# Performance work log

Hardware: AMD Instinct MI355X
Metric: run time of the kernel (lower is better)

The kernel has to match this reference:

```python
import math
import jax, jax.numpy as jnp
import numpy as np

B, S, D = 1, 2048, 2048
H, KV, HD = 32, 4, 64  # n_heads, n_kv_heads, head_dim
N_REP = H // KV
ROPE_THETA = 10000.0


def setup_inputs() -> dict:
    key = jax.random.key(0)
    ks = jax.random.split(key, 6)
    x = jax.random.normal(ks[0], (B, S, D), dtype=jnp.float32)
    # precomputed rotary frequencies (real/imag parts of freqs_cis)
    inv_freq = 1.0 / (ROPE_THETA ** (jnp.arange(0, HD, 2, dtype=jnp.float32) / HD))  # [HD/2]
    t = jnp.arange(S, dtype=jnp.float32)
    ang = jnp.outer(t, inv_freq)  # [S, HD/2]
    freqs_cos = jnp.cos(ang)
    freqs_sin = jnp.sin(ang)
    # additive causal mask (large negative instead of -inf; numerically equivalent)
    mask = jnp.where(jnp.tril(jnp.ones((S, S), dtype=bool)), 0.0, -1e9).astype(jnp.float32)
    scale = 0.02
    wq = jax.random.normal(ks[1], (D, H * HD), dtype=jnp.float32) * scale
    wk = jax.random.normal(ks[2], (D, KV * HD), dtype=jnp.float32) * scale
    wv = jax.random.normal(ks[3], (D, KV * HD), dtype=jnp.float32) * scale
    wo = jax.random.normal(ks[4], (H * HD, D), dtype=jnp.float32) * scale
    return {"x": x, "freqs_cos": freqs_cos, "freqs_sin": freqs_sin, "mask": mask,
            "wq": wq, "wk": wk, "wv": wv, "wo": wo}


def _rope(t, cos, sin):
    # t: [B,S,h,HD]; cos/sin: [S, HD/2] -> complex multiply on (even, odd) pairs
    tr = t.reshape(*t.shape[:-1], HD // 2, 2)
    t0, t1 = tr[..., 0], tr[..., 1]
    c = cos[None, :, None, :]
    s = sin[None, :, None, :]
    o0 = t0 * c - t1 * s
    o1 = t0 * s + t1 * c
    return jnp.stack([o0, o1], axis=-1).reshape(t.shape)


def reference(x, freqs_cos, freqs_sin, mask, wq, wk, wv, wo):
    bsz, seqlen, _ = x.shape
    xq = (x @ wq).reshape(bsz, seqlen, H, HD)
    xk = (x @ wk).reshape(bsz, seqlen, KV, HD)
    xv = (x @ wv).reshape(bsz, seqlen, KV, HD)
    xq = _rope(xq, freqs_cos, freqs_sin)
    xk = _rope(xk, freqs_cos, freqs_sin)
    # GQA: repeat kv heads
    xk = jnp.repeat(xk, N_REP, axis=2)  # [B,S,H,HD]
    xv = jnp.repeat(xv, N_REP, axis=2)
    scores = jnp.einsum('bqhd,bkhd->bhqk', xq, xk) / math.sqrt(HD)
    scores = scores + mask[None, None, :, :]
    probs = jax.nn.softmax(scores.astype(jnp.float32), axis=-1).astype(xq.dtype)
    out = jnp.einsum('bhqk,bkhd->bqhd', probs, xv).reshape(bsz, seqlen, H * HD)
    return out @ wo
```

## Files before the change

### kernel.cpp

```cpp
#include <hip/hip_runtime.h>

typedef unsigned short u16;
typedef __attribute__((ext_vector_type(4))) float f32x4;
typedef __attribute__((ext_vector_type(16))) float f32x16;
typedef __attribute__((ext_vector_type(8))) short bf16x8;
typedef __attribute__((ext_vector_type(4))) unsigned short u16x4;
typedef __attribute__((ext_vector_type(4))) unsigned u32x4;
typedef __attribute__((ext_vector_type(2))) unsigned uv2;

__device__ __forceinline__ u16 f2bf(float f) {
  unsigned u = __float_as_uint(f);
  u += 0x7FFFu + ((u >> 16) & 1u);
  return (u16)(u >> 16);
}
__device__ __forceinline__ float bf2f(u16 v) {
  return __uint_as_float(((unsigned)v) << 16);
}

__device__ __forceinline__ void gload_lds16(const u16* g, u16* l) {
  __builtin_amdgcn_global_load_lds((const __attribute__((address_space(1))) void*)g,
                                   (__attribute__((address_space(3))) void*)l, 16, 0, 0);
}

__device__ __forceinline__ unsigned cvt_pk_bf16(float lo, float hi) {
  unsigned r;
  asm("v_cvt_pk_bf16_f32 %0, %1, %2" : "=v"(r) : "v"(lo), "v"(hi));
  return r;
}

__device__ __forceinline__ float fexp2(float x) {
#if __has_builtin(__builtin_amdgcn_exp2f)
  return __builtin_amdgcn_exp2f(x);
#else
  return __expf(x * 0.6931471805599453f);
#endif
}

__global__ __launch_bounds__(256) void convert_f32_bf16(const float* __restrict__ in,
                                                        u16* __restrict__ out, int n) {
  int i = (blockIdx.x * 256 + threadIdx.x) * 4;
  if (i >= n) return;
  float4 v = *(const float4*)&in[i];
  out[i + 0] = f2bf(v.x);
  out[i + 1] = f2bf(v.y);
  out[i + 2] = f2bf(v.z);
  out[i + 3] = f2bf(v.w);
}

__global__ __launch_bounds__(256) void transpose_f32_bf16(const float* __restrict__ in,
                                                          u16* __restrict__ out,
                                                          int R, int C) {
  __shared__ float tile[32][33];
  int c0 = blockIdx.x * 32, r0 = blockIdx.y * 32;
  int tx = threadIdx.x, ty = threadIdx.y;
  for (int j = 0; j < 32; j += 8)
    tile[ty + j][tx] = in[(size_t)(r0 + ty + j) * C + c0 + tx];
  __syncthreads();
  for (int j = 0; j < 32; j += 8)
    out[(size_t)(c0 + ty + j) * R + r0 + tx] = f2bf(tile[tx][ty + j]);
}

__global__ __launch_bounds__(256) void transpose_wqkv(const float* __restrict__ wq,
                                                      const float* __restrict__ wk,
                                                      const float* __restrict__ wv,
                                                      u16* __restrict__ out) {
  __shared__ float tile[32][33];
  int bx = blockIdx.x, r0 = blockIdx.y * 32;
  const float* src;
  int C, cc0;
  if (bx < 64) { src = wq; C = 2048; cc0 = bx * 32; }
  else if (bx < 72) { src = wk; C = 256; cc0 = (bx - 64) * 32; }
  else { src = wv; C = 256; cc0 = (bx - 72) * 32; }
  int tx = threadIdx.x, ty = threadIdx.y;
  for (int j = 0; j < 32; j += 8)
    tile[ty + j][tx] = src[(size_t)(r0 + ty + j) * C + cc0 + tx];
  __syncthreads();
  for (int j = 0; j < 32; j += 8)
    out[(size_t)(bx * 32 + ty + j) * 2048 + r0 + tx] = f2bf(tile[tx][ty + j]);
}

__global__ __launch_bounds__(256) void transpose_bf16(const u16* __restrict__ in, int ld_in,
                                                      u16* __restrict__ out, int R, int C) {
  __shared__ u16 tile[32][33];
  int c0 = blockIdx.x * 32, r0 = blockIdx.y * 32;
  int tx = threadIdx.x, ty = threadIdx.y;
  for (int j = 0; j < 32; j += 8)
    tile[ty + j][tx] = in[(size_t)(r0 + ty + j) * ld_in + c0 + tx];
  __syncthreads();
  for (int j = 0; j < 32; j += 8)
    out[(size_t)(c0 + ty + j) * R + r0 + tx] = tile[tx][ty + j];
}

template <bool F32OUT, bool DO_ROPE>
__global__ __launch_bounds__(512, 4) void gemm_bt(const u16* __restrict__ A,
                                                  const u16* __restrict__ BT,
                                                  void* __restrict__ Cout,
                                                  int M, int N, int K,
                                                  const float* __restrict__ cosT,
                                                  const float* __restrict__ sinT) {
  const int bn = blockIdx.x * 128, bm = blockIdx.y * 128;
  const int tid = threadIdx.x;
  const int wid = tid >> 6, lane = tid & 63;
  const int wr = wid >> 2, wc = wid & 3;
  const int lrow = lane & 15, g = lane >> 4;

  __shared__ __align__(16) u16 As[2][128 * 64];
  __shared__ __align__(16) u16 Bs[2][128 * 64];

  const int srow = tid >> 3;
  const int cswz = (((tid & 7) ^ (srow & 7)) << 3);
  const u16* a_src = A + (size_t)(bm + srow) * K + cswz;
  const u16* b_src = BT + (size_t)(bn + srow) * K + cswz;

  const int swz16 = (lrow & 7) << 3;
  const int colsw0 = (g * 8) ^ swz16;
  const int colsw1 = (32 + g * 8) ^ swz16;

#define STAGE(buf, k0)                                                        \
  do {                                                                        \
    const u16* ap = a_src + (k0);                                             \
    const u16* bp = b_src + (k0);                                             \
    u16* ad = &As[buf][0] + tid * 8;                                          \
    u16* bd = &Bs[buf][0] + tid * 8;                                          \
    _Pragma("unroll") for (int p = 0; p < 2; ++p) {                           \
      gload_lds16(ap + (size_t)p * 64 * K, ad + p * 4096);                    \
      gload_lds16(bp + (size_t)p * 64 * K, bd + p * 4096);                    \
    }                                                                         \
  } while (0)

  f32x4 acc[4][2] = {};

  const int nt = K >> 6;
  STAGE(0, 0);
  int cur = 0;
  for (int t = 0; t < nt; ++t) {
    if (t + 1 < nt) {
      STAGE(cur ^ 1, (t + 1) * 64);
      asm volatile("s_waitcnt vmcnt(4)" ::: "memory");
    } else {
      asm volatile("s_waitcnt vmcnt(0)" ::: "memory");
    }
    __builtin_amdgcn_s_barrier();
    asm volatile("" ::: "memory");

    bf16x8 af[4][2], bfr[2][2];
#pragma unroll
    for (int m = 0; m < 4; ++m) {
      int row = wr * 64 + m * 16 + lrow;
      af[m][0] = *(const bf16x8*)&As[cur][row * 64 + colsw0];
      af[m][1] = *(const bf16x8*)&As[cur][row * 64 + colsw1];
    }
#pragma unroll
    for (int n = 0; n < 2; ++n) {
      int row = wc * 32 + n * 16 + lrow;
      bfr[n][0] = *(const bf16x8*)&Bs[cur][row * 64 + colsw0];
      bfr[n][1] = *(const bf16x8*)&Bs[cur][row * 64 + colsw1];
    }
#pragma unroll
    for (int ks = 0; ks < 2; ++ks)
#pragma unroll
      for (int m = 0; m < 4; ++m)
#pragma unroll
        for (int n = 0; n < 2; ++n)
          acc[m][n] =
              __builtin_amdgcn_mfma_f32_16x16x32_bf16(af[m][ks], bfr[n][ks], acc[m][n], 0, 0, 0);

    asm volatile("" ::: "memory");
    __builtin_amdgcn_s_barrier();
    cur ^= 1;
  }
#undef STAGE

#pragma unroll
  for (int m = 0; m < 4; ++m) {
    int row0 = bm + wr * 64 + m * 16 + (g << 2);
#pragma unroll
    for (int n = 0; n < 2; ++n) {
      int col = bn + wc * 32 + n * 16 + lrow;
      f32x4 v = acc[m][n];
      if constexpr (DO_ROPE) {
        if (bn < 2304) {
          int i = (col & 63) >> 1;
          float sg = (col & 1) ? 1.f : -1.f;
#pragma unroll
          for (int r = 0; r < 4; ++r) {
            float pv = __shfl_xor(v[r], 1, 64);
            float c = cosT[(row0 + r) * 32 + i];
            float s = sinT[(row0 + r) * 32 + i];
            v[r] = v[r] * c + pv * s * sg;
          }
        }
      }
#pragma unroll
      for (int r = 0; r < 4; ++r) {
        if constexpr (F32OUT)
          ((float*)Cout)[(size_t)(row0 + r) * N + col] = v[r];
        else
          ((u16*)Cout)[(size_t)(row0 + r) * N + col] = f2bf(v[r]);
      }
    }
  }
}

__global__ __launch_bounds__(512) void attn_kernel(const u16* __restrict__ QKV,
                                                   const u16* __restrict__ VT,
                                                   u16* __restrict__ attn_out) {
  const int h = blockIdx.x;
  const int qb = (int)gridDim.y - 1 - (int)blockIdx.y;
  const int tid = threadIdx.x, w = tid >> 6, lane = tid & 63;
  const int wq4 = w & 3, half = w >> 2;
  const int l31 = lane & 31, hh = lane >> 5;
  const int kh = h >> 3;
  const int q0w = qb * 128 + wq4 * 32;
  const int qg = q0w + l31;

  __shared__ __align__(16) u16 smem[32768];

  const int srow8 = lane >> 3;
  const int scol = (((lane & 7) ^ srow8) << 3);

#define ASTAGE(buf, kb)                                                              \
  do {                                                                               \
    u16* kd = smem + (half * 2 + (buf)) * 4096 + (wq4 * 8) * 64 + lane * 8;          \
    u16* vd = smem + 16384 + (half * 2 + (buf)) * 4096 + (wq4 * 8) * 64 + lane * 8;  \
    _Pragma("unroll") for (int p = 0; p < 2; ++p) {                                  \
      int rr = p * 32 + wq4 * 8 + srow8;                                             \
      gload_lds16(QKV + (size_t)((kb) + rr) * 2560 + 2048 + kh * 64 + scol,          \
                  kd + p * 2048);                                                    \
      gload_lds16(VT + (size_t)(kh * 64 + rr) * 2048 + (kb) + scol, vd + p * 2048);  \
    }                                                                                \
  } while (0)

  bf16x8 qf[4];
  {
    size_t base = (size_t)qg * 2560 + h * 64 + hh * 8;
#pragma unroll
    for (int ks = 0; ks < 4; ++ks) qf[ks] = *(const bf16x8*)&QKV[base + ks * 16];
  }

  const int ksw = (l31 & 7) << 3;

  f32x16 acc0 = {}, acc1 = {};
  float mrun = -1e30f, lrun = 0.f;
  const float SC = 0.125f * 1.44269504088896f;

  const int NT = qb + 1;
  ASTAGE(0, half * 64);
  int cur = 0;

  for (int t = 0; t < NT; ++t) {
    const int kb = (2 * t + half) * 64;
    if (t + 1 < NT) {
      ASTAGE(cur ^ 1, kb + 128);
      asm volatile("s_waitcnt vmcnt(4)" ::: "memory");
    } else {
      asm volatile("s_waitcnt vmcnt(0)" ::: "memory");
    }
    __builtin_amdgcn_s_barrier();
    asm volatile("" ::: "memory");

    if (kb <= q0w + 31) {
      const u16* Kc = smem + (half * 2 + cur) * 4096;
      const u16* Vc = smem + 16384 + (half * 2 + cur) * 4096;

      f32x16 sc0 = {}, sc1 = {};
      __builtin_amdgcn_s_setprio(1);
#pragma unroll
      for (int ks = 0; ks < 4; ++ks) {
        int c = (ks * 16 + hh * 8) ^ ksw;
        bf16x8 kf0 = *(const bf16x8*)&Kc[l31 * 64 + c];
        bf16x8 kf1 = *(const bf16x8*)&Kc[(32 + l31) * 64 + c];
        sc0 = __builtin_amdgcn_mfma_f32_32x32x16_bf16(kf0, qf[ks], sc0, 0, 0, 0);
        sc1 = __builtin_amdgcn_mfma_f32_32x32x16_bf16(kf1, qf[ks], sc1, 0, 0, 0);
      }
      __builtin_amdgcn_s_setprio(0);

      if (kb + 63 > q0w) {
#pragma unroll
        for (int r = 0; r < 16; ++r) {
          int keyoff = (r & 3) + 8 * (r >> 2) + 4 * hh;
          if (kb + keyoff > qg) sc0[r] = -1e5f;
          if (kb + 32 + keyoff > qg) sc1[r] = -1e5f;
        }
      }

      float m8[8];
#pragma unroll
      for (int i = 0; i < 8; ++i)
        m8[i] = fmaxf(fmaxf(sc0[i], sc0[i + 8]), fmaxf(sc1[i], sc1[i + 8]));
#pragma unroll
      for (int st = 4; st >= 1; st >>= 1)
#pragma unroll
        for (int i = 0; i < st; ++i) m8[i] = fmaxf(m8[i], m8[i + st]);
      float mx = fmaxf(m8[0], __shfl_xor(m8[0], 32, 64));
      float mxs = mx * SC;

      if (__any(mxs > mrun + 8.f)) {
        float nm = fmaxf(mrun, mxs);
        float fs = fexp2(mrun - nm);
        mrun = nm;
        lrun *= fs;
#pragma unroll
        for (int i = 0; i < 16; ++i) { acc0[i] *= fs; acc1[i] *= fs; }
      }

      float p0[16], p1[16];
      const float nmn = -mrun;
#pragma unroll
      for (int i = 0; i < 16; ++i) {
        p0[i] = fexp2(__builtin_fmaf(sc0[i], SC, nmn));
        p1[i] = fexp2(__builtin_fmaf(sc1[i], SC, nmn));
      }
      float s8[8];
#pragma unroll
      for (int i = 0; i < 8; ++i) s8[i] = (p0[i] + p0[i + 8]) + (p1[i] + p1[i + 8]);
#pragma unroll
      for (int st = 4; st >= 1; st >>= 1)
#pragma unroll
        for (int i = 0; i < st; ++i) s8[i] += s8[i + st];
      lrun += s8[0] + __shfl_xor(s8[0], 32, 64);

      bf16x8 pf[4];
#pragma unroll
      for (int tt = 0; tt < 2; ++tt) {
        const float* pp = tt ? p1 : p0;
        unsigned wd[8];
#pragma unroll
        for (int j = 0; j < 8; ++j) wd[j] = cvt_pk_bf16(pp[2 * j], pp[2 * j + 1]);
        uv2 sA = __builtin_amdgcn_permlane32_swap(wd[0], wd[2], false, false);
        uv2 sB = __builtin_amdgcn_permlane32_swap(wd[1], wd[3], false, false);
        uv2 sC = __builtin_amdgcn_permlane32_swap(wd[4], wd[6], false, false);
        uv2 sD = __builtin_amdgcn_permlane32_swap(wd[5], wd[7], false, false);
        u32x4 f0 = {sA[0], sB[0], sA[1], sB[1]};
        u32x4 f1 = {sC[0], sD[0], sC[1], sD[1]};
        pf[tt * 2 + 0] = __builtin_bit_cast(bf16x8, f0);
        pf[tt * 2 + 1] = __builtin_bit_cast(bf16x8, f1);
      }

      __builtin_amdgcn_s_setprio(1);
#pragma unroll
      for (int ks = 0; ks < 4; ++ks) {
        int c = (ks * 16 + hh * 8) ^ ksw;
        bf16x8 vf0 = *(const bf16x8*)&Vc[l31 * 64 + c];
        bf16x8 vf1 = *(const bf16x8*)&Vc[(32 + l31) * 64 + c];
        acc0 = __builtin_amdgcn_mfma_f32_32x32x16_bf16(vf0, pf[ks], acc0, 0, 0, 0);
        acc1 = __builtin_amdgcn_mfma_f32_32x32x16_bf16(vf1, pf[ks], acc1, 0, 0, 0);
      }
      __builtin_amdgcn_s_setprio(0);
    }

    asm volatile("" ::: "memory");
    __builtin_amdgcn_s_barrier();
    cur ^= 1;
  }
#undef ASTAGE

  float* MRG = (float*)smem;
  float4* CH = (float4*)smem;
  if (half == 1) {
#pragma unroll
    for (int c = 0; c < 4; ++c) {
      float4 v0 = {acc0[4 * c + 0], acc0[4 * c + 1], acc0[4 * c + 2], acc0[4 * c + 3]};
      float4 v1 = {acc1[4 * c + 0], acc1[4 * c + 1], acc1[4 * c + 2], acc1[4 * c + 3]};
      CH[(wq4 * 8 + c) * 64 + lane] = v0;
      CH[(wq4 * 8 + 4 + c) * 64 + lane] = v1;
    }
    MRG[8192 + wq4 * 128 + lane * 2 + 0] = mrun;
    MRG[8192 + wq4 * 128 + lane * 2 + 1] = lrun;
  }
  __syncthreads();
  if (half == 0) {
    float m1 = MRG[8192 + wq4 * 128 + lane * 2 + 0];
    float l1 = MRG[8192 + wq4 * 128 + lane * 2 + 1];
    float m = fmaxf(mrun, m1);
    float f0 = fexp2(mrun - m), f1 = fexp2(m1 - m);
    float inv = 1.f / (lrun * f0 + l1 * f1);
    float a = f0 * inv, b = f1 * inv;
    size_t obase = (size_t)qg * 2048 + h * 64;
#pragma unroll
    for (int c = 0; c < 4; ++c) {
      float4 r0 = CH[(wq4 * 8 + c) * 64 + lane];
      float4 r1 = CH[(wq4 * 8 + 4 + c) * 64 + lane];
      u16x4 o0, o1;
      o0[0] = f2bf(acc0[4 * c + 0] * a + r0.x * b);
      o0[1] = f2bf(acc0[4 * c + 1] * a + r0.y * b);
      o0[2] = f2bf(acc0[4 * c + 2] * a + r0.z * b);
      o0[3] = f2bf(acc0[4 * c + 3] * a + r0.w * b);
      o1[0] = f2bf(acc1[4 * c + 0] * a + r1.x * b);
      o1[1] = f2bf(acc1[4 * c + 1] * a + r1.y * b);
      o1[2] = f2bf(acc1[4 * c + 2] * a + r1.z * b);
      o1[3] = f2bf(acc1[4 * c + 3] * a + r1.w * b);
      *(u16x4*)&attn_out[obase + 8 * c + 4 * hh] = o0;
      *(u16x4*)&attn_out[obase + 32 + 8 * c + 4 * hh] = o1;
    }
  }
}

extern "C" void kernel_launch(void* const* d_in, const int* in_sizes, int n_in,
                              void* d_out, int out_size, void* d_ws, size_t ws_size,
                              hipStream_t stream) {
  const float* x = (const float*)d_in[0];
  const float* fcos = (const float*)d_in[1];
  const float* fsin = (const float*)d_in[2];
  const float* wq = (const float*)d_in[4];
  const float* wk = (const float*)d_in[5];
  const float* wv = (const float*)d_in[6];
  const float* wo = (const float*)d_in[7];

  char* ws = (char*)d_ws;
  u16* xb    = (u16*)(ws);
  u16* wqkvT = (u16*)(ws + (8u << 20));
  u16* woT   = (u16*)(ws + (18u << 20));
  u16* QKV   = (u16*)(ws + (26u << 20));
  u16* VT    = (u16*)(ws + (36u << 20));
  u16* attn  = xb;

  dim3 tb32(32, 8);

  convert_f32_bf16<<<4096, 256, 0, stream>>>(x, xb, 2048 * 2048);
  transpose_wqkv<<<dim3(80, 64), tb32, 0, stream>>>(wq, wk, wv, wqkvT);
  transpose_f32_bf16<<<dim3(64, 64), tb32, 0, stream>>>(wo, woT, 2048, 2048);

  gemm_bt<false, true><<<dim3(20, 16), 512, 0, stream>>>(xb, wqkvT, QKV, 2048, 2560, 2048,
                                                         fcos, fsin);

  transpose_bf16<<<dim3(8, 64), tb32, 0, stream>>>(QKV + 2304, 2560, VT, 2048, 256);

  attn_kernel<<<dim3(32, 16), 512, 0, stream>>>(QKV, VT, attn);

  gemm_bt<true, false><<<dim3(16, 16), 512, 0, stream>>>(attn, woT, d_out, 2048, 2048, 2048,
                                                         nullptr, nullptr);
}
```

Before: 126.7 us.

## Balance causal attention work by splitting long query blocks across paired workgroups

```diff
diff --git a/kernel.cpp b/kernel.cpp
--- a/kernel.cpp
+++ b/kernel.cpp
@@ -204,195 +204,253 @@
 
 __global__ __launch_bounds__(512) void attn_kernel(const u16* __restrict__ QKV,
                                                    const u16* __restrict__ VT,
-                                                   u16* __restrict__ attn_out) {
+                                                   u16* __restrict__ attn_out,
+                                                   u16* __restrict__ Ppart) {
   const int h = blockIdx.x;
-  const int qb = (int)gridDim.y - 1 - (int)blockIdx.y;
+  const int p = blockIdx.y & 7, piece = blockIdx.y >> 3;
   const int tid = threadIdx.x, w = tid >> 6, lane = tid & 63;
   const int wq4 = w & 3, half = w >> 2;
   const int l31 = lane & 31, hh = lane >> 5;
   const int kh = h >> 3;
-  const int q0w = qb * 128 + wq4 * 32;
-  const int qg = q0w + l31;
 
   __shared__ __align__(16) u16 smem[32768];
 
   const int srow8 = lane >> 3;
   const int scol = (((lane & 7) ^ srow8) << 3);
+  const int ksw = (l31 & 7) << 3;
+  const float SC = 0.125f * 1.44269504088896f;
 
 #define ASTAGE(buf, kb)                                                              \
   do {                                                                               \
     u16* kd = smem + (half * 2 + (buf)) * 4096 + (wq4 * 8) * 64 + lane * 8;          \
     u16* vd = smem + 16384 + (half * 2 + (buf)) * 4096 + (wq4 * 8) * 64 + lane * 8;  \
-    _Pragma("unroll") for (int p = 0; p < 2; ++p) {                                  \
-      int rr = p * 32 + wq4 * 8 + srow8;                                             \
+    _Pragma("unroll") for (int pp = 0; pp < 2; ++pp) {                               \
+      int rr = pp * 32 + wq4 * 8 + srow8;                                            \
       gload_lds16(QKV + (size_t)((kb) + rr) * 2560 + 2048 + kh * 64 + scol,          \
-                  kd + p * 2048);                                                    \
-      gload_lds16(VT + (size_t)(kh * 64 + rr) * 2048 + (kb) + scol, vd + p * 2048);  \
+                  kd + pp * 2048);                                                   \
+      gload_lds16(VT + (size_t)(kh * 64 + rr) * 2048 + (kb) + scol, vd + pp * 2048); \
     }                                                                                \
   } while (0)
 
-  bf16x8 qf[4];
-  {
-    size_t base = (size_t)qg * 2560 + h * 64 + hh * 8;
-#pragma unroll
-    for (int ks = 0; ks < 4; ++ks) qf[ks] = *(const bf16x8*)&QKV[base + ks * 16];
-  }
-
-  const int ksw = (l31 & 7) << 3;
-
-  f32x16 acc0 = {}, acc1 = {};
-  float mrun = -1e30f, lrun = 0.f;
-  const float SC = 0.125f * 1.44269504088896f;
-
-  const int NT = qb + 1;
-  ASTAGE(0, half * 64);
-  int cur = 0;
-
-  for (int t = 0; t < NT; ++t) {
-    const int kb = (2 * t + half) * 64;
-    if (t + 1 < NT) {
-      ASTAGE(cur ^ 1, kb + 128);
-      asm volatile("s_waitcnt vmcnt(4)" ::: "memory");
-    } else {
-      asm volatile("s_waitcnt vmcnt(0)" ::: "memory");
-    }
-    __builtin_amdgcn_s_barrier();
-    asm volatile("" ::: "memory");
-
-    if (kb <= q0w + 31) {
-      const u16* Kc = smem + (half * 2 + cur) * 4096;
-      const u16* Vc = smem + 16384 + (half * 2 + cur) * 4096;
-
-      f32x16 sc0 = {}, sc1 = {};
-      __builtin_amdgcn_s_setprio(1);
-#pragma unroll
-      for (int ks = 0; ks < 4; ++ks) {
-        int c = (ks * 16 + hh * 8) ^ ksw;
-        bf16x8 kf0 = *(const bf16x8*)&Kc[l31 * 64 + c];
-        bf16x8 kf1 = *(const bf16x8*)&Kc[(32 + l31) * 64 + c];
-        sc0 = __builtin_amdgcn_mfma_f32_32x32x16_bf16(kf0, qf[ks], sc0, 0, 0, 0);
-        sc1 = __builtin_amdgcn_mfma_f32_32x32x16_bf16(kf1, qf[ks], sc1, 0, 0, 0);
-      }
-      __builtin_amdgcn_s_setprio(0);
-
-      if (kb + 63 > q0w) {
-#pragma unroll
-        for (int r = 0; r < 16; ++r) {
-          int keyoff = (r & 3) + 8 * (r >> 2) + 4 * hh;
-          if (kb + keyoff > qg) sc0[r] = -1e5f;
-          if (kb + 32 + keyoff > qg) sc1[r] = -1e5f;
-        }
-      }
-
-      float m8[8];
-#pragma unroll
-      for (int i = 0; i < 8; ++i)
-        m8[i] = fmaxf(fmaxf(sc0[i], sc0[i + 8]), fmaxf(sc1[i], sc1[i + 8]));
-#pragma unroll
-      for (int st = 4; st >= 1; st >>= 1)
-#pragma unroll
-        for (int i = 0; i < st; ++i) m8[i] = fmaxf(m8[i], m8[i + st]);
-      float mx = fmaxf(m8[0], __shfl_xor(m8[0], 32, 64));
-      float mxs = mx * SC;
-
-      if (__any(mxs > mrun + 8.f)) {
-        float nm = fmaxf(mrun, mxs);
-        float fs = fexp2(mrun - nm);
-        mrun = nm;
-        lrun *= fs;
-#pragma unroll
-        for (int i = 0; i < 16; ++i) { acc0[i] *= fs; acc1[i] *= fs; }
-      }
-
-      float p0[16], p1[16];
-      const float nmn = -mrun;
-#pragma unroll
-      for (int i = 0; i < 16; ++i) {
-        p0[i] = fexp2(__builtin_fmaf(sc0[i], SC, nmn));
-        p1[i] = fexp2(__builtin_fmaf(sc1[i], SC, nmn));
-      }
-      float s8[8];
-#pragma unroll
-      for (int i = 0; i < 8; ++i) s8[i] = (p0[i] + p0[i + 8]) + (p1[i] + p1[i + 8]);
-#pragma unroll
-      for (int st = 4; st >= 1; st >>= 1)
-#pragma unroll
-        for (int i = 0; i < st; ++i) s8[i] += s8[i + st];
-      lrun += s8[0] + __shfl_xor(s8[0], 32, 64);
-
-      bf16x8 pf[4];
-#pragma unroll
-      for (int tt = 0; tt < 2; ++tt) {
-        const float* pp = tt ? p1 : p0;
-        unsigned wd[8];
-#pragma unroll
-        for (int j = 0; j < 8; ++j) wd[j] = cvt_pk_bf16(pp[2 * j], pp[2 * j + 1]);
-        uv2 sA = __builtin_amdgcn_permlane32_swap(wd[0], wd[2], false, false);
-        uv2 sB = __builtin_amdgcn_permlane32_swap(wd[1], wd[3], false, false);
-        uv2 sC = __builtin_amdgcn_permlane32_swap(wd[4], wd[6], false, false);
-        uv2 sD = __builtin_amdgcn_permlane32_swap(wd[5], wd[7], false, false);
-        u32x4 f0 = {sA[0], sB[0], sA[1], sB[1]};
-        u32x4 f1 = {sC[0], sD[0], sC[1], sD[1]};
-        pf[tt * 2 + 0] = __builtin_bit_cast(bf16x8, f0);
-        pf[tt * 2 + 1] = __builtin_bit_cast(bf16x8, f1);
-      }
-
-      __builtin_amdgcn_s_setprio(1);
-#pragma unroll
-      for (int ks = 0; ks < 4; ++ks) {
-        int c = (ks * 16 + hh * 8) ^ ksw;
-        bf16x8 vf0 = *(const bf16x8*)&Vc[l31 * 64 + c];
-        bf16x8 vf1 = *(const bf16x8*)&Vc[(32 + l31) * 64 + c];
-        acc0 = __builtin_amdgcn_mfma_f32_32x32x16_bf16(vf0, pf[ks], acc0, 0, 0, 0);
-        acc1 = __builtin_amdgcn_mfma_f32_32x32x16_bf16(vf1, pf[ks], acc1, 0, 0, 0);
-      }
-      __builtin_amdgcn_s_setprio(0);
-    }
-
-    asm volatile("" ::: "memory");
-    __builtin_amdgcn_s_barrier();
-    cur ^= 1;
+  auto do_phase = [&](int qb, int t0, int t1, bool finalW, int pidx) {
+    const int q0w = qb * 128 + wq4 * 32;
+    const int qg = q0w + l31;
+
+    __syncthreads();
+
+    bf16x8 qf[4];
+    {
+      size_t base = (size_t)qg * 2560 + h * 64 + hh * 8;
+#pragma unroll
+      for (int ks = 0; ks < 4; ++ks) qf[ks] = *(const bf16x8*)&QKV[base + ks * 16];
+    }
+
+    f32x16 acc0 = {}, acc1 = {};
+    float mrun = -1e30f, lrun = 0.f;
+
+    ASTAGE(0, (2 * t0 + half) * 64);
+    int cur = 0;
+
+    for (int t = t0; t < t1; ++t) {
+      const int kb = (2 * t + half) * 64;
+      if (t + 1 < t1) {
+        ASTAGE(cur ^ 1, kb + 128);
+        asm volatile("s_waitcnt vmcnt(4)" ::: "memory");
+      } else {
+        asm volatile("s_waitcnt vmcnt(0)" ::: "memory");
+      }
+      __builtin_amdgcn_s_barrier();
+      asm volatile("" ::: "memory");
+
+      if (kb <= q0w + 31) {
+        const u16* Kc = smem + (half * 2 + cur) * 4096;
+        const u16* Vc = smem + 16384 + (half * 2 + cur) * 4096;
+
+        f32x16 sc0 = {}, sc1 = {};
+        __builtin_amdgcn_s_setprio(1);
+#pragma unroll
+        for (int ks = 0; ks < 4; ++ks) {
+          int c = (ks * 16 + hh * 8) ^ ksw;
+          bf16x8 kf0 = *(const bf16x8*)&Kc[l31 * 64 + c];
+          bf16x8 kf1 = *(const bf16x8*)&Kc[(32 + l31) * 64 + c];
+          sc0 = __builtin_amdgcn_mfma_f32_32x32x16_bf16(kf0, qf[ks], sc0, 0, 0, 0);
+          sc1 = __builtin_amdgcn_mfma_f32_32x32x16_bf16(kf1, qf[ks], sc1, 0, 0, 0);
+        }
+        __builtin_amdgcn_s_setprio(0);
+
+        if (kb + 63 > q0w) {
+#pragma unroll
+          for (int r = 0; r < 16; ++r) {
+            int keyoff = (r & 3) + 8 * (r >> 2) + 4 * hh;
+            if (kb + keyoff > qg) sc0[r] = -1e5f;
+            if (kb + 32 + keyoff > qg) sc1[r] = -1e5f;
+          }
+        }
+
+        float m8[8];
+#pragma unroll
+        for (int i = 0; i < 8; ++i)
+          m8[i] = fmaxf(fmaxf(sc0[i], sc0[i + 8]), fmaxf(sc1[i], sc1[i + 8]));
+#pragma unroll
+        for (int st = 4; st >= 1; st >>= 1)
+#pragma unroll
+          for (int i = 0; i < st; ++i) m8[i] = fmaxf(m8[i], m8[i + st]);
+        float mx = fmaxf(m8[0], __shfl_xor(m8[0], 32, 64));
+        float mxs = mx * SC;
+
+        if (__any(mxs > mrun + 8.f)) {
+          float nm = fmaxf(mrun, mxs);
+          float fs = fexp2(mrun - nm);
+          mrun = nm;
+          lrun *= fs;
+#pragma unroll
+          for (int i = 0; i < 16; ++i) { acc0[i] *= fs; acc1[i] *= fs; }
+        }
+
+        float p0[16], p1[16];
+        const float nmn = -mrun;
+#pragma unroll
+        for (int i = 0; i < 16; ++i) {
+          p0[i] = fexp2(__builtin_fmaf(sc0[i], SC, nmn));
+          p1[i] = fexp2(__builtin_fmaf(sc1[i], SC, nmn));
+        }
+        float s8[8];
+#pragma unroll
+        for (int i = 0; i < 8; ++i) s8[i] = (p0[i] + p0[i + 8]) + (p1[i] + p1[i + 8]);
+#pragma unroll
+        for (int st = 4; st >= 1; st >>= 1)
+#pragma unroll
+          for (int i = 0; i < st; ++i) s8[i] += s8[i + st];
+        lrun += s8[0] + __shfl_xor(s8[0], 32, 64);
+
+        bf16x8 pf[4];
+#pragma unroll
+        for (int tt = 0; tt < 2; ++tt) {
+          const float* pp = tt ? p1 : p0;
+          unsigned wd[8];
+#pragma unroll
+          for (int j = 0; j < 8; ++j) wd[j] = cvt_pk_bf16(pp[2 * j], pp[2 * j + 1]);
+          uv2 sA = __builtin_amdgcn_permlane32_swap(wd[0], wd[2], false, false);
+          uv2 sB = __builtin_amdgcn_permlane32_swap(wd[1], wd[3], false, false);
+          uv2 sC = __builtin_amdgcn_permlane32_swap(wd[4], wd[6], false, false);
+          uv2 sD = __builtin_amdgcn_permlane32_swap(wd[5], wd[7], false, false);
+          u32x4 f0 = {sA[0], sB[0], sA[1], sB[1]};
+          u32x4 f1 = {sC[0], sD[0], sC[1], sD[1]};
+          pf[tt * 2 + 0] = __builtin_bit_cast(bf16x8, f0);
+          pf[tt * 2 + 1] = __builtin_bit_cast(bf16x8, f1);
+        }
+
+        __builtin_amdgcn_s_setprio(1);
+#pragma unroll
+        for (int ks = 0; ks < 4; ++ks) {
+          int c = (ks * 16 + hh * 8) ^ ksw;
+          bf16x8 vf0 = *(const bf16x8*)&Vc[l31 * 64 + c];
+          bf16x8 vf1 = *(const bf16x8*)&Vc[(32 + l31) * 64 + c];
+          acc0 = __builtin_amdgcn_mfma_f32_32x32x16_bf16(vf0, pf[ks], acc0, 0, 0, 0);
+          acc1 = __builtin_amdgcn_mfma_f32_32x32x16_bf16(vf1, pf[ks], acc1, 0, 0, 0);
+        }
+        __builtin_amdgcn_s_setprio(0);
+      }
+
+      asm volatile("" ::: "memory");
+      __builtin_amdgcn_s_barrier();
+      cur ^= 1;
+    }
+
+    float* MRG = (float*)smem;
+    float4* CH = (float4*)smem;
+    if (half == 1) {
+#pragma unroll
+      for (int c = 0; c < 4; ++c) {
+        float4 v0 = {acc0[4 * c + 0], acc0[4 * c + 1], acc0[4 * c + 2], acc0[4 * c + 3]};
+        float4 v1 = {acc1[4 * c + 0], acc1[4 * c + 1], acc1[4 * c + 2], acc1[4 * c + 3]};
+        CH[(wq4 * 8 + c) * 64 + lane] = v0;
+        CH[(wq4 * 8 + 4 + c) * 64 + lane] = v1;
+      }
+      MRG[8192 + wq4 * 128 + lane * 2 + 0] = mrun;
+      MRG[8192 + wq4 * 128 + lane * 2 + 1] = lrun;
+    }
+    __syncthreads();
+    if (half == 0) {
+      float m1 = MRG[8192 + wq4 * 128 + lane * 2 + 0];
+      float l1 = MRG[8192 + wq4 * 128 + lane * 2 + 1];
+      float m = fmaxf(mrun, m1);
+      float f0 = fexp2(mrun - m), f1 = fexp2(m1 - m);
+      float a, b;
+      u16* obase;
+      size_t ostride;
+      if (finalW) {
+        float inv = 1.f / (lrun * f0 + l1 * f1);
+        a = f0 * inv; b = f1 * inv;
+        obase = attn_out + (size_t)qg * 2048 + h * 64;
+        ostride = 1;
+      } else {
+        a = f0; b = f1;
+        u16* pb = Ppart + (size_t)((h * 8 + p) * 2 + pidx) * 8704;
+        obase = pb + (wq4 * 32 + l31) * 64;
+        ostride = 1;
+        if (hh == 0) {
+          float* pm = (float*)(pb + 8192);
+          pm[wq4 * 32 + l31] = m;
+          pm[128 + wq4 * 32 + l31] = lrun * f0 + l1 * f1;
+        }
+      }
+#pragma unroll
+      for (int c = 0; c < 4; ++c) {
+        float4 r0 = CH[(wq4 * 8 + c) * 64 + lane];
+        float4 r1 = CH[(wq4 * 8 + 4 + c) * 64 + lane];
+        u16x4 o0, o1;
+        o0[0] = f2bf(acc0[4 * c + 0] * a + r0.x * b);
+        o0[1] = f2bf(acc0[4 * c + 1] * a + r0.y * b);
+        o0[2] = f2bf(acc0[4 * c + 2] * a + r0.z * b);
+        o0[3] = f2bf(acc0[4 * c + 3] * a + r0.w * b);
+        o1[0] = f2bf(acc1[4 * c + 0] * a + r1.x * b);
+        o1[1] = f2bf(acc1[4 * c + 1] * a + r1.y * b);
+        o1[2] = f2bf(acc1[4 * c + 2] * a + r1.z * b);
+        o1[3] = f2bf(acc1[4 * c + 3] * a + r1.w * b);
+        *(u16x4*)&obase[8 * c + 4 * hh] = o0;
+        *(u16x4*)&obase[32 + 8 * c + 4 * hh] = o1;
+      }
+    }
+  };
+
+  if (piece == 0) {
+    do_phase(p, 0, p + 1, true, -1);
+    if (p < 7) do_phase(15 - p, 0, 7 - p, false, 0);
+  } else {
+    const int t0 = 7 - p;
+    do_phase(15 - p, t0, 16 - p, t0 == 0, 1);
   }
 #undef ASTAGE
-
-  float* MRG = (float*)smem;
-  float4* CH = (float4*)smem;
-  if (half == 1) {
-#pragma unroll
-    for (int c = 0; c < 4; ++c) {
-      float4 v0 = {acc0[4 * c + 0], acc0[4 * c + 1], acc0[4 * c + 2], acc0[4 * c + 3]};
-      float4 v1 = {acc1[4 * c + 0], acc1[4 * c + 1], acc1[4 * c + 2], acc1[4 * c + 3]};
-      CH[(wq4 * 8 + c) * 64 + lane] = v0;
-      CH[(wq4 * 8 + 4 + c) * 64 + lane] = v1;
-    }
-    MRG[8192 + wq4 * 128 + lane * 2 + 0] = mrun;
-    MRG[8192 + wq4 * 128 + lane * 2 + 1] = lrun;
-  }
-  __syncthreads();
-  if (half == 0) {
-    float m1 = MRG[8192 + wq4 * 128 + lane * 2 + 0];
-    float l1 = MRG[8192 + wq4 * 128 + lane * 2 + 1];
-    float m = fmaxf(mrun, m1);
-    float f0 = fexp2(mrun - m), f1 = fexp2(m1 - m);
-    float inv = 1.f / (lrun * f0 + l1 * f1);
-    float a = f0 * inv, b = f1 * inv;
-    size_t obase = (size_t)qg * 2048 + h * 64;
-#pragma unroll
-    for (int c = 0; c < 4; ++c) {
-      float4 r0 = CH[(wq4 * 8 + c) * 64 + lane];
-      float4 r1 = CH[(wq4 * 8 + 4 + c) * 64 + lane];
-      u16x4 o0, o1;
-      o0[0] = f2bf(acc0[4 * c + 0] * a + r0.x * b);
-      o0[1] = f2bf(acc0[4 * c + 1] * a + r0.y * b);
-      o0[2] = f2bf(acc0[4 * c + 2] * a + r0.z * b);
-      o0[3] = f2bf(acc0[4 * c + 3] * a + r0.w * b);
-      o1[0] = f2bf(acc1[4 * c + 0] * a + r1.x * b);
-      o1[1] = f2bf(acc1[4 * c + 1] * a + r1.y * b);
-      o1[2] = f2bf(acc1[4 * c + 2] * a + r1.z * b);
-      o1[3] = f2bf(acc1[4 * c + 3] * a + r1.w * b);
-      *(u16x4*)&attn_out[obase + 8 * c + 4 * hh] = o0;
-      *(u16x4*)&attn_out[obase + 32 + 8 * c + 4 * hh] = o1;
-    }
+}
+
+__global__ __launch_bounds__(256) void attn_merge(const u16* __restrict__ Ppart,
+                                                  u16* __restrict__ attn_out) {
+  const int h = blockIdx.x, p = blockIdx.y;
+  const int b = 15 - p;
+  const int tid = threadIdx.x;
+  const int r = tid >> 1, dh = tid & 1;
+  const u16* b0 = Ppart + (size_t)((h * 8 + p) * 2 + 0) * 8704;
+  const u16* b1 = Ppart + (size_t)((h * 8 + p) * 2 + 1) * 8704;
+  const float* ml0 = (const float*)(b0 + 8192);
+  const float* ml1 = (const float*)(b1 + 8192);
+  float m0 = ml0[r], l0 = ml0[128 + r];
+  float m1 = ml1[r], l1 = ml1[128 + r];
+  float m = fmaxf(m0, m1);
+  float f0 = fexp2(m0 - m), f1 = fexp2(m1 - m);
+  float inv = 1.f / (l0 * f0 + l1 * f1);
+  float a = f0 * inv, bs = f1 * inv;
+  const u16* a0 = b0 + r * 64 + dh * 32;
+  const u16* a1 = b1 + r * 64 + dh * 32;
+  u16* out = attn_out + (size_t)(b * 128 + r) * 2048 + h * 64 + dh * 32;
+#pragma unroll
+  for (int j = 0; j < 8; ++j) {
+    u16x4 v0 = *(const u16x4*)&a0[j * 4];
+    u16x4 v1 = *(const u16x4*)&a1[j * 4];
+    u16x4 o;
+#pragma unroll
+    for (int e = 0; e < 4; ++e) o[e] = f2bf(bf2f(v0[e]) * a + bf2f(v1[e]) * bs);
+    *(u16x4*)&out[j * 4] = o;
   }
 }
 
@@ -414,6 +472,7 @@
   u16* QKV   = (u16*)(ws + (26u << 20));
   u16* VT    = (u16*)(ws + (36u << 20));
   u16* attn  = xb;
+  u16* Ppart = wqkvT;
 
   dim3 tb32(32, 8);
 
@@ -426,7 +485,8 @@
 
   transpose_bf16<<<dim3(8, 64), tb32, 0, stream>>>(QKV + 2304, 2560, VT, 2048, 256);
 
-  attn_kernel<<<dim3(32, 16), 512, 0, stream>>>(QKV, VT, attn);
+  attn_kernel<<<dim3(32, 16), 512, 0, stream>>>(QKV, VT, attn, Ppart);
+  attn_merge<<<dim3(32, 7), 256, 0, stream>>>(Ppart, attn);
 
   gemm_bt<true, false><<<dim3(16, 16), 512, 0, stream>>>(attn, woT, d_out, 2048, 2048, 2048,
                                                          nullptr, nullptr);
```

Result: slower. 134.5 us (+6.2%).
